# Performance work log

Measured on AMD Instinct MI355X. Metric: run time of the kernel, lower is better.

The kernel has to match this reference:

```python
import jax, jax.numpy as jnp
import numpy as np

VOCAB = 31
SOS = 0  # VOCAB_MAP['<sos>']
B, T_ENC, T_DEC, D = 64, 1000, 300, 512


def setup_inputs() -> dict:
    key = jax.random.key(0)
    ks = jax.random.split(key, 18)
    s = 0.05
    n = lambda k, shp: jax.random.normal(k, shp, jnp.float32) * s
    return {
        "encoder_output": jax.random.normal(ks[0], (B, T_ENC, D), jnp.float32),
        "encoder_len": jax.random.randint(ks[1], (B,), 100, T_ENC + 1),
        "y": jax.random.randint(ks[2], (B, T_DEC), 0, VOCAB),
        "embedding": n(ks[3], (VOCAB, D)),
        "W_ih0": n(ks[4], (4 * D, 2 * D)),
        "W_hh0": n(ks[5], (4 * D, D)),
        "b_ih0": jnp.zeros((4 * D,), jnp.float32),
        "b_hh0": jnp.zeros((4 * D,), jnp.float32),
        "W_ih1": n(ks[6], (4 * D, D)),
        "W_hh1": n(ks[7], (4 * D, D)),
        "b_ih1": jnp.zeros((4 * D,), jnp.float32),
        "b_hh1": jnp.zeros((4 * D,), jnp.float32),
        "Wq": n(ks[8], (D, D)),
        "Wk": n(ks[9], (D, D)),
        "Wv": n(ks[10], (D, D)),
        "W_out": n(ks[11], (D, 2 * D)),
        "b_out": jnp.zeros((D,), jnp.float32),
        "b_char": jnp.zeros((VOCAB,), jnp.float32),
    }


def _lstm_cell(x, h, c, Wih, Whh, bih, bhh):
    # torch LSTMCell: gates = x@Wih^T + bih + h@Whh^T + bhh, chunk order i,f,g,o
    g = x @ Wih.T + bih + h @ Whh.T + bhh
    i, f, gg, o = jnp.split(g, 4, axis=-1)
    c2 = jax.nn.sigmoid(f) * c + jax.nn.sigmoid(i) * jnp.tanh(gg)
    h2 = jax.nn.sigmoid(o) * jnp.tanh(c2)
    return h2, c2


def reference(encoder_output, encoder_len, y, embedding, W_ih0, W_hh0, b_ih0,
              b_hh0, W_ih1, W_hh1, b_ih1, b_hh1, Wq, Wk, Wv, W_out, b_out,
              b_char):
    Bb, T_dec = y.shape
    T_enc = encoder_output.shape[1]
    Dd = embedding.shape[1]
    # precompute attention keys/values once (attender caches these)
    keys_ = encoder_output @ Wk   # [B, T_enc, D]
    vals_ = encoder_output @ Wv   # [B, T_enc, D]
    mask = jnp.arange(T_enc)[None, :] < encoder_len[:, None]  # [B, T_enc]
    scale = 1.0 / jnp.sqrt(jnp.asarray(Dd, jnp.float32))

    def step(carry, xs):
        h0, c0, h1, c1, ctx, prev = carry
        t, yt = xs
        # teacher forcing (ratio=1): y[:,t] for 0<t<T-1, else previous argmax
        sym = jnp.where((t > 0) & (t < T_dec - 1), yt, prev)
        emb = embedding[sym]                       # [B, D]
        x = jnp.concatenate([emb, ctx], axis=-1)   # [B, 2D]
        h0, c0 = _lstm_cell(x, h0, c0, W_ih0, W_hh0, b_ih0, b_hh0)
        h1, c1 = _lstm_cell(h0, h1, c1, W_ih1, W_hh1, b_ih1, b_hh1)
        q = h1 @ Wq                                # [B, D]
        e = jnp.einsum('bd,btd->bt', q, keys_) * scale
        e = jnp.where(mask, e, jnp.float32(-1e9))
        w = jax.nn.softmax(e, axis=-1)             # [B, T_enc]
        ctx = jnp.einsum('bt,btd->bd', w, vals_)   # [B, D]
        cdn = jnp.concatenate([h1, ctx], axis=-1)  # [B, 2D]
        hid = jax.nn.relu(cdn @ W_out.T + b_out)
        logits = hid @ embedding.T + b_char        # tied weights, [B, 31]
        prev = jnp.argmax(logits, axis=-1)
        return (h0, c0, h1, c1, ctx, prev), (logits, w)

    z = jnp.zeros((Bb, Dd), encoder_output.dtype)
    prev0 = jnp.full((Bb,), SOS, dtype=y.dtype)
    init = (z, z, z, z, z, prev0)
    ts = jnp.arange(T_dec)
    _, (logits, attn) = jax.lax.scan(step, init, (ts, y.T))
    raw_outputs = jnp.transpose(logits, (1, 0, 2))      # [B, T_dec, 31]
    attention_plot = jnp.transpose(attn, (1, 0, 2))     # [B, T_dec, T_enc]
    return raw_outputs, attention_plot
```

## Files before the change

kernel.cpp:

```cpp
#include <hip/hip_runtime.h>


typedef __attribute__((ext_vector_type(8))) short s8bf;
typedef __attribute__((ext_vector_type(4))) float f32x4;

#define SCALE_E 0.044194173824159216f
#define SWEEP_SLOTS 352
#define POLL_CAP 65536

struct Ptrs {
  const float* enc; const int* elen; const int* y;
  const float* emb;
  const float* Wih0; const float* Whh0; const float* bih0; const float* bhh0;
  const float* Wih1; const float* Whh1; const float* bih1; const float* bhh1;
  const float* Wq; const float* Wk; const float* Wv;
  const float* Wout; const float* bout; const float* bchar;
  unsigned short* kv;
  unsigned short* W0p;
  unsigned short* W1p;
  unsigned short* Wob;
  unsigned short* WkvT;
  unsigned short* embbf;
  float* b0p; float* b1p;
  unsigned short* h0b;
  unsigned short* h1b;
  unsigned short* hidb;
  unsigned short* embsel;
  float* c0s; float* c1s;
  float* ctxa;
  float* ebuf;
  float* sbuf;
  int* plan;
  int* flagA;
  float* out;
};

__device__ __forceinline__ unsigned short f2bf(float f) {
  unsigned u = __float_as_uint(f);
  u += 0x7fffu + ((u >> 16) & 1u);
  return (unsigned short)(u >> 16);
}
__device__ __forceinline__ float bf2f(unsigned short h) {
  return __uint_as_float(((unsigned)h) << 16);
}
__device__ __forceinline__ float sigm(float x) { return 1.f / (1.f + __expf(-x)); }

__device__ __forceinline__ void st_u32_sc(unsigned* p, unsigned v) {
  __hip_atomic_store(p, v, __ATOMIC_RELAXED, __HIP_MEMORY_SCOPE_AGENT);
}
__device__ __forceinline__ s8bf ld16_sc(const unsigned short* p) {
  union { unsigned long long u[2]; s8bf v; } w;
  w.u[0] = __hip_atomic_load((unsigned long long*)p, __ATOMIC_RELAXED,
                             __HIP_MEMORY_SCOPE_AGENT);
  w.u[1] = __hip_atomic_load((unsigned long long*)(p + 4), __ATOMIC_RELAXED,
                             __HIP_MEMORY_SCOPE_AGENT);
  return w.v;
}

__global__ void k_init(Ptrs P) {
  int g = blockIdx.x * 256 + threadIdx.x;
  for (int i = g; i < 32768; i += 65536) { P.c0s[i] = 0.f; P.c1s[i] = 0.f; }
  for (int i = g; i < 65536; i += 65536) {
    P.h0b[i] = 0; P.h1b[i] = 0; P.ctxa[i] = 0.f;
  }
  for (int i = g; i < 131072; i += 65536) P.ebuf[i] = 0.f;
  if (g < 128) P.sbuf[g] = 0.f;
  if (g < 64) P.flagA[g] = 0;
}

__global__ void k_prep(Ptrs P) {
  int bid = blockIdx.x, tid = threadIdx.x;
  for (int ri = 0; ri < 8; ++ri) {
    int gp = bid * 8 + ri;
    int r = (gp & 3) * 512 + (gp >> 2);
    for (int k = tid; k < 1536; k += 256)
      P.W0p[(size_t)gp * 1536 + k] =
          f2bf(k < 1024 ? P.Wih0[(size_t)r * 1024 + k] : P.Whh0[(size_t)r * 512 + (k - 1024)]);
    for (int k = tid; k < 1024; k += 256)
      P.W1p[(size_t)gp * 1024 + k] =
          f2bf(k < 512 ? P.Wih1[(size_t)r * 512 + k] : P.Whh1[(size_t)r * 512 + (k - 512)]);
    if (tid == 0) {
      P.b0p[gp] = P.bih0[r] + P.bhh0[r];
      P.b1p[gp] = P.bih1[r] + P.bhh1[r];
    }
  }
  for (int ri = 0; ri < 2; ++ri) {
    int n = bid * 2 + ri;
    for (int k = tid; k < 1024; k += 256)
      P.Wob[(size_t)n * 1024 + k] = f2bf(P.Wout[(size_t)n * 1024 + k]);
  }
  {
    int g = bid * 256 + tid;
    if (g < 31 * 512) P.embbf[g] = f2bf(P.emb[g]);
  }
  for (int ri = 0; ri < 4; ++ri) {
    int n = bid * 4 + ri;
    if (n < 512) {
      const float* wq = P.Wq + (size_t)n * 512;
      for (int k = tid; k < 512; k += 256) {
        const float* wk = P.Wk + (size_t)k * 512;
        float s0 = 0.f, s1 = 0.f, s2 = 0.f, s3 = 0.f;
        for (int j = 0; j < 512; j += 4) {
          f32x4 a = *(const f32x4*)(wk + j);
          f32x4 b = *(const f32x4*)(wq + j);
          s0 = fmaf(a[0], b[0], s0); s1 = fmaf(a[1], b[1], s1);
          s2 = fmaf(a[2], b[2], s2); s3 = fmaf(a[3], b[3], s3);
        }
        P.WkvT[(size_t)n * 512 + k] = f2bf((s0 + s1) + (s2 + s3));
      }
    } else {
      for (int k = tid; k < 512; k += 256)
        P.WkvT[(size_t)n * 512 + k] = f2bf(P.Wv[(size_t)k * 512 + (n - 512)]);
    }
  }
  if (bid == 0 && tid == 0) {
    int tot = 0;
    for (int b = 0; b < 64; ++b) {
      int l = P.elen[b]; if (l > 1000) l = 1000;
      tot += l;
    }
    int acc = 0;
    P.plan[0] = 0;
    for (int b = 0; b < 64; ++b) {
      int l = P.elen[b]; if (l > 1000) l = 1000;
      int nb = (int)(((long long)l * 288) / tot);
      if (nb < 1) nb = 1;
      acc += nb;
      P.plan[b + 1] = acc;
    }
  }
}

__global__ __launch_bounds__(1024) void k_kv(Ptrs P) {
  int bid = blockIdx.x, tid = threadIdx.x;
  int w = tid >> 6, ln = tid & 63;
  __shared__ unsigned short lds2[16][16][16];
  int mt = bid * 16 + w;
  bool valid = mt < 4000;
  s8bf afr[16];
  if (valid) {
    const float* ar = P.enc + (size_t)(mt * 16 + (ln & 15)) * 512 + ((ln >> 4) * 8);
    for (int ks = 0; ks < 16; ++ks) {
      f32x4 v0 = *(const f32x4*)(ar + ks * 32);
      f32x4 v1 = *(const f32x4*)(ar + ks * 32 + 4);
      s8bf a;
      a[0] = (short)f2bf(v0[0]); a[1] = (short)f2bf(v0[1]);
      a[2] = (short)f2bf(v0[2]); a[3] = (short)f2bf(v0[3]);
      a[4] = (short)f2bf(v1[0]); a[5] = (short)f2bf(v1[1]);
      a[6] = (short)f2bf(v1[2]); a[7] = (short)f2bf(v1[3]);
      afr[ks] = a;
    }
  }
  for (int nt = 0; nt < 64; ++nt) {
    if (valid) {
      f32x4 acc = {0.f, 0.f, 0.f, 0.f};
      const unsigned short* br = P.WkvT + (size_t)(nt * 16 + (ln & 15)) * 512 + ((ln >> 4) * 8);
      for (int ks = 0; ks < 16; ++ks) {
        s8bf b = *(const s8bf*)(br + ks * 32);
        acc = __builtin_amdgcn_mfma_f32_16x16x32_bf16(afr[ks], b, acc, 0, 0, 0);
      }
      for (int r = 0; r < 4; ++r)
        lds2[w][(ln >> 4) * 4 + r][ln & 15] = f2bf(acc[r]);
    }
    __syncthreads();
    if (valid && ln < 32) {
      int row = ln >> 1, half = ln & 1;
      s8bf v = *(const s8bf*)&lds2[w][row][half * 8];
      *(s8bf*)(P.kv + (size_t)(mt * 16 + row) * 1024 + nt * 16 + half * 8) = v;
    }
    __syncthreads();
  }
}

__device__ __forceinline__ void hid_phase(int j, int tid, int s, const Ptrs& P,
                                          float (*lds_g)[16][16]) {
  int w = tid >> 6, ln = tid & 63;
  int kq = w >> 2, mt = w & 3;
  int nt = j;
  int brow = mt * 16 + (ln & 15), koff = (ln >> 4) * 8;
  int par = s & 1;
  const unsigned short* bp = P.Wob + (size_t)(nt * 16 + (ln & 15)) * 1024 + kq * 512 + koff;
  f32x4 acc = {0.f, 0.f, 0.f, 0.f};
  if (kq == 0) {
    const unsigned short* ap = P.h1b + par * 32768 + (size_t)brow * 512 + koff;
    for (int ks = 0; ks < 16; ++ks) {
      s8bf af = *(const s8bf*)(ap + ks * 32);
      s8bf bf8 = *(const s8bf*)(bp + ks * 32);
      acc = __builtin_amdgcn_mfma_f32_16x16x32_bf16(af, bf8, acc, 0, 0, 0);
    }
  } else {
    float inv = 1.f / P.sbuf[par * 64 + brow];
    const float* ap = P.ctxa + par * 32768 + (size_t)brow * 512 + koff;
    for (int ks = 0; ks < 16; ++ks) {
      f32x4 v0 = *(const f32x4*)(ap + ks * 32);
      f32x4 v1 = *(const f32x4*)(ap + ks * 32 + 4);
      s8bf af;
      af[0] = (short)f2bf(v0[0] * inv); af[1] = (short)f2bf(v0[1] * inv);
      af[2] = (short)f2bf(v0[2] * inv); af[3] = (short)f2bf(v0[3] * inv);
      af[4] = (short)f2bf(v1[0] * inv); af[5] = (short)f2bf(v1[1] * inv);
      af[6] = (short)f2bf(v1[2] * inv); af[7] = (short)f2bf(v1[3] * inv);
      s8bf bf8 = *(const s8bf*)(bp + ks * 32);
      acc = __builtin_amdgcn_mfma_f32_16x16x32_bf16(af, bf8, acc, 0, 0, 0);
    }
  }
  for (int r = 0; r < 4; ++r)
    lds_g[w][(ln >> 4) * 4 + r][ln & 15] = acc[r];
  __syncthreads();
  for (int r = 0; r < 2; ++r) {
    int idx = r * 512 + tid;
    int mt2 = idx >> 8, rb = (idx >> 4) & 15, cc = idx & 15;
    float hsum = lds_g[mt2][rb][cc] + lds_g[4 + mt2][rb][cc];
    hsum += P.bout[nt * 16 + cc];
    hsum = fmaxf(hsum, 0.f);
    P.hidb[(size_t)(mt2 * 16 + rb) * 512 + nt * 16 + cc] = f2bf(hsum);
  }
}

__device__ __forceinline__ void logits_phase(int lb, int tid, int s, const Ptrs& P,
                                             bool do_argmax) {
  int w = tid >> 6, ln = tid & 63;
  if (w >= 8) return;
  int b = lb * 8 + w;
  float hv[8];
  s8bf hh = *(const s8bf*)(P.hidb + (size_t)b * 512 + ln * 8);
  for (int j = 0; j < 8; ++j) hv[j] = bf2f((unsigned short)hh[j]);
  float mx = -3.4e38f; int am = 0;
  for (int v = 0; v < 31; ++v) {
    s8bf ee = *(const s8bf*)(P.embbf + (size_t)v * 512 + ln * 8);
    float p = 0.f;
    for (int j = 0; j < 8; ++j) p = fmaf(bf2f((unsigned short)ee[j]), hv[j], p);
    for (int off = 32; off; off >>= 1) p += __shfl_down(p, off);
    if (ln == 0) {
      float lg = p + P.bchar[v];
      P.out[(size_t)b * 9300 + (size_t)s * 31 + v] = lg;
      if (lg > mx) { mx = lg; am = v; }
    }
  }
  if (do_argmax) {
    am = __shfl(am, 0);
    *(s8bf*)(P.embsel + (size_t)b * 512 + ln * 8) =
        *(const s8bf*)(P.embbf + (size_t)am * 512 + ln * 8);
  }
}

__device__ __forceinline__ void attnnorm_phase(int j, int tid, int s, const Ptrs& P) {
  int idx = j * 512 + tid;
  if (idx >= 16000) return;
  int b = idx / 250, r = idx - b * 250;
  int par = s & 1;
  float inv = 1.f / P.sbuf[par * 64 + b];
  f32x4 v = *(const f32x4*)(P.ebuf + par * 65536 + b * 1024 + r * 4);
  v[0] *= inv; v[1] *= inv; v[2] *= inv; v[3] *= inv;
  *(f32x4*)(P.out + 595200 + (size_t)b * 300000 + (size_t)s * 1000 + r * 4) = v;
}

__global__ __launch_bounds__(512) void k_AB(Ptrs P, int t, int do_hid) {
  __shared__ float lds_g[8][16][16];
  __shared__ unsigned short lds_h0[16][520];
  int bid = blockIdx.x, tid = threadIdx.x;

  if (bid < 64) {
    int g = bid >> 4, s = bid & 15;
    int w = tid >> 6, ln = tid & 63;
    int nt = s * 8 + w;
    int brow = g * 16 + (ln & 15);
    int koff = (ln >> 4) * 8;
    int cur = t & 1, prv = cur ^ 1;

    const unsigned short* bp = P.W0p + (size_t)(nt * 16 + (ln & 15)) * 1536 + koff;
    f32x4 acc = {0.f, 0.f, 0.f, 0.f};
    {
      const unsigned short* embrow;
      if (t == 299) {
        embrow = P.embsel + (size_t)brow * 512 + koff;
      } else {
        int sym = (t == 0) ? 0 : P.y[brow * 300 + t];
        embrow = P.embbf + (size_t)sym * 512 + koff;
      }
      for (int ks = 0; ks < 16; ++ks) {
        s8bf af = *(const s8bf*)(embrow + ks * 32);
        s8bf bf8 = *(const s8bf*)(bp + ks * 32);
        acc = __builtin_amdgcn_mfma_f32_16x16x32_bf16(af, bf8, acc, 0, 0, 0);
      }
    }
    if (t > 0) {
      float inv = 1.f / P.sbuf[prv * 64 + brow];
      const float* cp = P.ctxa + prv * 32768 + (size_t)brow * 512 + koff;
      for (int ks = 0; ks < 16; ++ks) {
        f32x4 v0 = *(const f32x4*)(cp + ks * 32);
        f32x4 v1 = *(const f32x4*)(cp + ks * 32 + 4);
        s8bf af;
        af[0] = (short)f2bf(v0[0] * inv); af[1] = (short)f2bf(v0[1] * inv);
        af[2] = (short)f2bf(v0[2] * inv); af[3] = (short)f2bf(v0[3] * inv);
        af[4] = (short)f2bf(v1[0] * inv); af[5] = (short)f2bf(v1[1] * inv);
        af[6] = (short)f2bf(v1[2] * inv); af[7] = (short)f2bf(v1[3] * inv);
        s8bf bf8 = *(const s8bf*)(bp + 512 + ks * 32);
        acc = __builtin_amdgcn_mfma_f32_16x16x32_bf16(af, bf8, acc, 0, 0, 0);
      }
    }
    {
      const unsigned short* hp = P.h0b + prv * 32768 + (size_t)brow * 512 + koff;
      for (int ks = 0; ks < 16; ++ks) {
        s8bf af = *(const s8bf*)(hp + ks * 32);
        s8bf bf8 = *(const s8bf*)(bp + 1024 + ks * 32);
        acc = __builtin_amdgcn_mfma_f32_16x16x32_bf16(af, bf8, acc, 0, 0, 0);
      }
    }
    {
      float bias = P.b0p[nt * 16 + (ln & 15)];
      for (int r = 0; r < 4; ++r)
        lds_g[w][(ln >> 4) * 4 + r][ln & 15] = acc[r] + bias;
    }
    __syncthreads();
    {
      int tile = tid >> 6, rb = (tid >> 2) & 15, c = tid & 3;
      float gi = lds_g[tile][rb][4 * c + 0];
      float gf = lds_g[tile][rb][4 * c + 1];
      float gg = lds_g[tile][rb][4 * c + 2];
      float go = lds_g[tile][rb][4 * c + 3];
      int bb = g * 16 + rb, d = (s * 8 + tile) * 4 + c;
      float co = P.c0s[bb * 512 + d];
      float cn = fmaf(sigm(gf), co, sigm(gi) * tanhf(gg));
      float h = sigm(go) * tanhf(cn);
      P.c0s[bb * 512 + d] = cn;
      unsigned short hb = f2bf(h);
      int pr = __shfl_xor((int)(unsigned)hb, 1);
      if ((tid & 1) == 0)
        st_u32_sc((unsigned*)(P.h0b + cur * 32768 + bb * 512 + d),
                  ((unsigned)hb) | ((unsigned)pr << 16));
    }
    __syncthreads();

    if (tid == 0) {
      __hip_atomic_fetch_add(P.flagA + g * 16, 1, __ATOMIC_RELAXED,
                             __HIP_MEMORY_SCOPE_AGENT);
      int target = 16 * (t + 1);
      int gc = 0;
      while (__hip_atomic_load(P.flagA + g * 16, __ATOMIC_RELAXED,
                               __HIP_MEMORY_SCOPE_AGENT) < target) {
        if (++gc > POLL_CAP) break;
        __builtin_amdgcn_s_sleep(1);
      }
    }
    __syncthreads();

    {
      int bb2 = tid >> 5;
      int c0 = (tid & 31) * 16;
      const unsigned short* src = P.h0b + cur * 32768 + (size_t)(g * 16 + bb2) * 512 + c0;
      s8bf v0 = ld16_sc(src);
      s8bf v1 = ld16_sc(src + 8);
      *(s8bf*)&lds_h0[bb2][c0] = v0;
      *(s8bf*)&lds_h0[bb2][c0 + 8] = v1;
    }
    __syncthreads();

    const unsigned short* bp1 = P.W1p + (size_t)(nt * 16 + (ln & 15)) * 1024 + koff;
    f32x4 acc1 = {0.f, 0.f, 0.f, 0.f};
    for (int ks = 0; ks < 16; ++ks) {
      s8bf af = *(const s8bf*)&lds_h0[ln & 15][koff + ks * 32];
      s8bf bf8 = *(const s8bf*)(bp1 + ks * 32);
      acc1 = __builtin_amdgcn_mfma_f32_16x16x32_bf16(af, bf8, acc1, 0, 0, 0);
    }
    {
      const unsigned short* h1p = P.h1b + prv * 32768 + (size_t)brow * 512 + koff;
      for (int ks = 0; ks < 16; ++ks) {
        s8bf af = *(const s8bf*)(h1p + ks * 32);
        s8bf bf8 = *(const s8bf*)(bp1 + 512 + ks * 32);
        acc1 = __builtin_amdgcn_mfma_f32_16x16x32_bf16(af, bf8, acc1, 0, 0, 0);
      }
    }
    {
      float bias = P.b1p[nt * 16 + (ln & 15)];
      for (int r = 0; r < 4; ++r)
        lds_g[w][(ln >> 4) * 4 + r][ln & 15] = acc1[r] + bias;
    }
    __syncthreads();
    {
      int tile = tid >> 6, rb = (tid >> 2) & 15, c = tid & 3;
      float gi = lds_g[tile][rb][4 * c + 0];
      float gf = lds_g[tile][rb][4 * c + 1];
      float gg = lds_g[tile][rb][4 * c + 2];
      float go = lds_g[tile][rb][4 * c + 3];
      int bb = g * 16 + rb, d = (s * 8 + tile) * 4 + c;
      float co = P.c1s[bb * 512 + d];
      float cn = fmaf(sigm(gf), co, sigm(gi) * tanhf(gg));
      float h = sigm(go) * tanhf(cn);
      P.c1s[bb * 512 + d] = cn;
      unsigned short hb = f2bf(h);
      int pr = __shfl_xor((int)(unsigned)hb, 1);
      if ((tid & 1) == 0)
        *(unsigned*)(P.h1b + cur * 32768 + bb * 512 + d) =
            ((unsigned)hb) | ((unsigned)pr << 16);
    }
  } else if (bid < 96) {
    if (t > 0 && do_hid) hid_phase(bid - 64, tid, t - 1, P, lds_g);
  } else if (bid < 128) {
    if (t > 0) attnnorm_phase(bid - 96, tid, t - 1, P);
  } else {
    int idx = (bid - 128) * 512 + tid;
    f32x4 z = {0.f, 0.f, 0.f, 0.f};
    *(f32x4*)(P.ctxa + (t & 1) * 32768 + idx * 4) = z;
    if (bid == 128 && tid < 64) P.sbuf[(t & 1) * 64 + tid] = 0.f;
  }
}

__global__ __launch_bounds__(1024) void k_C(Ptrs P, int t, int do_logits) {
  __shared__ float lds_ctx[16][512];
  __shared__ float lds_s[16];
  __shared__ int lplan[65];
  int bid = blockIdx.x, tid = threadIdx.x;
  if (bid >= SWEEP_SLOTS) {
    if (do_logits) logits_phase(bid - SWEEP_SLOTS, tid, t - 1, P, false);
    return;
  }
  if (tid < 65) lplan[tid] = P.plan[tid];
  __syncthreads();
  if (bid >= lplan[64]) return;
  int lo = 0, hi = 64;
  while (lo + 1 < hi) { int mid = (lo + hi) >> 1; if (bid >= lplan[mid]) lo = mid; else hi = mid; }
  int b = lo;
  int nb = lplan[b + 1] - lplan[b];
  int ci = bid - lplan[b];
  int len = P.elen[b]; if (len > 1000) len = 1000;
  int per = (len + nb - 1) / nb;
  int t0 = ci * per;
  int lim = t0 + per; if (lim > len) lim = len;
  if (t0 >= lim) return;

  int w = tid >> 6, ln = tid & 63;
  int par = t & 1;
  float h1r[8];
  {
    s8bf hh = *(const s8bf*)(P.h1b + par * 32768 + (size_t)b * 512 + ln * 8);
    for (int j = 0; j < 8; ++j) h1r[j] = bf2f((unsigned short)hh[j]);
  }
  float acc[8] = {0.f, 0.f, 0.f, 0.f, 0.f, 0.f, 0.f, 0.f};
  float wsum = 0.f;
  float* eb = P.ebuf + par * 65536 + b * 1024;
  const unsigned short* kvb = P.kv + (size_t)b * 1000 * 1024;
  int tt = t0 + w;
  s8bf k0, v0, k1, v1;
  bool hv0 = tt < lim, hv1 = (tt + 16) < lim;
  if (hv0) {
    const unsigned short* r = kvb + (size_t)tt * 1024 + ln * 8;
    k0 = *(const s8bf*)r; v0 = *(const s8bf*)(r + 512);
  }
  if (hv1) {
    const unsigned short* r = kvb + (size_t)(tt + 16) * 1024 + ln * 8;
    k1 = *(const s8bf*)r; v1 = *(const s8bf*)(r + 512);
  }
  while (hv0) {
    s8bf k2, v2;
    bool hv2 = (tt + 32) < lim;
    if (hv2) {
      const unsigned short* r = kvb + (size_t)(tt + 32) * 1024 + ln * 8;
      k2 = *(const s8bf*)r; v2 = *(const s8bf*)(r + 512);
    }
    float p0 = 0.f, p1 = 0.f;
    for (int j = 0; j < 8; j += 2) {
      p0 = fmaf(bf2f((unsigned short)k0[j]), h1r[j], p0);
      p1 = fmaf(bf2f((unsigned short)k0[j + 1]), h1r[j + 1], p1);
    }
    float p = p0 + p1;
    p += __shfl_xor(p, 32); p += __shfl_xor(p, 16); p += __shfl_xor(p, 8);
    p += __shfl_xor(p, 4);  p += __shfl_xor(p, 2);  p += __shfl_xor(p, 1);
    float pe = __expf(p * SCALE_E);
    if (ln == 0) { eb[tt] = pe; wsum += pe; }
    for (int j = 0; j < 8; ++j)
      acc[j] = fmaf(bf2f((unsigned short)v0[j]), pe, acc[j]);
    k0 = k1; v0 = v1; hv0 = hv1;
    k1 = k2; v1 = v2; hv1 = hv2;
    tt += 16;
  }
  if (ln == 0) lds_s[w] = wsum;
  for (int j = 0; j < 8; ++j) lds_ctx[w][ln * 8 + j] = acc[j];
  __syncthreads();
  if (tid < 512) {
    float s = 0.f;
    for (int i = 0; i < 16; ++i) s += lds_ctx[i][tid];
    unsafeAtomicAdd(P.ctxa + par * 32768 + b * 512 + tid, s);
  }
  if (tid == 0) {
    float s = 0.f;
    for (int i = 0; i < 16; ++i) s += lds_s[i];
    unsafeAtomicAdd(P.sbuf + par * 64 + b, s);
  }
}

__global__ __launch_bounds__(512) void k_hid(Ptrs P, int t) {
  __shared__ float lds_g[8][16][16];
  hid_phase(blockIdx.x, threadIdx.x, t, P, lds_g);
}
__global__ __launch_bounds__(512) void k_logits(Ptrs P, int t, int do_argmax) {
  logits_phase(blockIdx.x, threadIdx.x, t, P, do_argmax != 0);
}
__global__ __launch_bounds__(512) void k_attn(Ptrs P, int t) {
  attnnorm_phase(blockIdx.x, threadIdx.x, t, P);
}

extern "C" void kernel_launch(void* const* d_in, const int* in_sizes, int n_in,
                              void* d_out, int out_size, void* d_ws, size_t ws_size,
                              hipStream_t stream) {
  (void)in_sizes; (void)n_in; (void)out_size; (void)ws_size;
  Ptrs P;
  P.enc   = (const float*)d_in[0];
  P.elen  = (const int*)d_in[1];
  P.y     = (const int*)d_in[2];
  P.emb   = (const float*)d_in[3];
  P.Wih0  = (const float*)d_in[4];
  P.Whh0  = (const float*)d_in[5];
  P.bih0  = (const float*)d_in[6];
  P.bhh0  = (const float*)d_in[7];
  P.Wih1  = (const float*)d_in[8];
  P.Whh1  = (const float*)d_in[9];
  P.bih1  = (const float*)d_in[10];
  P.bhh1  = (const float*)d_in[11];
  P.Wq    = (const float*)d_in[12];
  P.Wk    = (const float*)d_in[13];
  P.Wv    = (const float*)d_in[14];
  P.Wout  = (const float*)d_in[15];
  P.bout  = (const float*)d_in[16];
  P.bchar = (const float*)d_in[17];
  P.out   = (float*)d_out;

  char* ws = (char*)d_ws;
  size_t o = 0;
  auto alloc = [&](size_t n) { char* p = ws + o; o = (o + n + 255) & ~(size_t)255; return p; };
  P.kv     = (unsigned short*)alloc(64000ull * 1024 * 2);
  P.W0p    = (unsigned short*)alloc(2048ull * 1536 * 2);
  P.W1p    = (unsigned short*)alloc(2048ull * 1024 * 2);
  P.Wob    = (unsigned short*)alloc(512ull * 1024 * 2);
  P.WkvT   = (unsigned short*)alloc(1024ull * 512 * 2);
  P.embbf  = (unsigned short*)alloc(31ull * 512 * 2);
  P.b0p    = (float*)alloc(2048 * 4);
  P.b1p    = (float*)alloc(2048 * 4);
  P.h0b    = (unsigned short*)alloc(2ull * 64 * 512 * 2);
  P.h1b    = (unsigned short*)alloc(2ull * 64 * 512 * 2);
  P.hidb   = (unsigned short*)alloc(64ull * 512 * 2);
  P.embsel = (unsigned short*)alloc(64ull * 512 * 2);
  P.c0s    = (float*)alloc(64ull * 512 * 4);
  P.c1s    = (float*)alloc(64ull * 512 * 4);
  P.ctxa   = (float*)alloc(2ull * 64 * 512 * 4);
  P.ebuf   = (float*)alloc(2ull * 64 * 1024 * 4);
  P.sbuf   = (float*)alloc(2ull * 64 * 4);
  P.plan   = (int*)alloc(65 * 4);
  P.flagA  = (int*)alloc(64 * 4);

  k_init<<<dim3(256), dim3(256), 0, stream>>>(P);
  k_prep<<<dim3(256), dim3(256), 0, stream>>>(P);
  k_kv<<<dim3(256), dim3(1024), 0, stream>>>(P);

  for (int t = 0; t < 300; ++t) {
    k_AB<<<dim3(144), dim3(512), 0, stream>>>(P, t, (t == 299) ? 0 : 1);
    k_C<<<dim3(SWEEP_SLOTS + 8), dim3(1024), 0, stream>>>(
        P, t, (t > 0 && t != 299) ? 1 : 0);
    if (t == 298) {
      k_hid<<<dim3(32), dim3(512), 0, stream>>>(P, 298);
      k_logits<<<dim3(8), dim3(512), 0, stream>>>(P, 298, 1);
    }
  }
  k_hid<<<dim3(32), dim3(512), 0, stream>>>(P, 299);
  k_attn<<<dim3(32), dim3(512), 0, stream>>>(P, 299);
  k_logits<<<dim3(8), dim3(512), 0, stream>>>(P, 299, 0);
}
```

Measured before the change: 20.85 ms.

## Fuse per-step LSTM and attention sweep into one kernel with flag sync

Merges the two per-timestep launches (LSTM/hid block and attention sweep with logits) into a single 512-block kernel. Cross-block dependencies are now handled by device-scope flag polling: flagH gates the attention sweep on the h1 write, and flagHid gates logits on the hid write. Context/sum zeroing moves into the LSTM blocks, and attention blocks shrink to 512 threads with more slots. The aim is to halve launch overhead and let phases overlap, at the cost of spin-waiting blocks that rely on co-residency. Polls that hit the cap break out and could read stale data.

```diff
diff --git a/kernel.cpp b/kernel.cpp
--- a/kernel.cpp
+++ b/kernel.cpp
@@ -5,8 +5,8 @@
 typedef __attribute__((ext_vector_type(4))) float f32x4;
 
 #define SCALE_E 0.044194173824159216f
-#define SWEEP_SLOTS 352
-#define POLL_CAP 65536
+#define SWEEP_SLOTS 376
+#define POLL_CAP (1 << 19)
 
 struct Ptrs {
   const float* enc; const int* elen; const int* y;
@@ -31,7 +31,9 @@
   float* ebuf;
   float* sbuf;
   int* plan;
-  int* flagA;
+  int* flagL;
+  int* flagH;
+  int* flagHid;
   float* out;
 };
 
@@ -46,6 +48,9 @@
 __device__ __forceinline__ float sigm(float x) { return 1.f / (1.f + __expf(-x)); }
 
 __device__ __forceinline__ void st_u32_sc(unsigned* p, unsigned v) {
+  __hip_atomic_store(p, v, __ATOMIC_RELAXED, __HIP_MEMORY_SCOPE_AGENT);
+}
+__device__ __forceinline__ void st_f32_sc(float* p, float v) {
   __hip_atomic_store(p, v, __ATOMIC_RELAXED, __HIP_MEMORY_SCOPE_AGENT);
 }
 __device__ __forceinline__ s8bf ld16_sc(const unsigned short* p) {
@@ -56,6 +61,14 @@
                              __HIP_MEMORY_SCOPE_AGENT);
   return w.v;
 }
+__device__ __forceinline__ void pollge(const int* p, int need) {
+  int g = 0;
+  while (__hip_atomic_load((int*)p, __ATOMIC_RELAXED, __HIP_MEMORY_SCOPE_AGENT) < need) {
+    if (++g > POLL_CAP) break;
+    if (g < 16) __builtin_amdgcn_s_sleep(1);
+    else        __builtin_amdgcn_s_sleep(8);
+  }
+}
 
 __global__ void k_init(Ptrs P) {
   int g = blockIdx.x * 256 + threadIdx.x;
@@ -65,7 +78,8 @@
   }
   for (int i = g; i < 131072; i += 65536) P.ebuf[i] = 0.f;
   if (g < 128) P.sbuf[g] = 0.f;
-  if (g < 64) P.flagA[g] = 0;
+  if (g < 64) { P.flagL[g] = 0; P.flagH[g] = 0; }
+  if (g < 16) P.flagHid[g] = 0;
 }
 
 __global__ void k_prep(Ptrs P) {
@@ -123,7 +137,7 @@
     P.plan[0] = 0;
     for (int b = 0; b < 64; ++b) {
       int l = P.elen[b]; if (l > 1000) l = 1000;
-      int nb = (int)(((long long)l * 288) / tot);
+      int nb = (int)(((long long)l * 312) / tot);
       if (nb < 1) nb = 1;
       acc += nb;
       P.plan[b + 1] = acc;
@@ -212,7 +226,11 @@
     float hsum = lds_g[mt2][rb][cc] + lds_g[4 + mt2][rb][cc];
     hsum += P.bout[nt * 16 + cc];
     hsum = fmaxf(hsum, 0.f);
-    P.hidb[(size_t)(mt2 * 16 + rb) * 512 + nt * 16 + cc] = f2bf(hsum);
+    unsigned short hb = f2bf(hsum);
+    int pr = __shfl_xor((int)(unsigned)hb, 1);
+    if ((tid & 1) == 0)
+      st_u32_sc((unsigned*)(P.hidb + (size_t)(mt2 * 16 + rb) * 512 + nt * 16 + cc),
+                ((unsigned)hb) | ((unsigned)pr << 16));
   }
 }
 
@@ -222,7 +240,7 @@
   if (w >= 8) return;
   int b = lb * 8 + w;
   float hv[8];
-  s8bf hh = *(const s8bf*)(P.hidb + (size_t)b * 512 + ln * 8);
+  s8bf hh = ld16_sc(P.hidb + (size_t)b * 512 + ln * 8);
   for (int j = 0; j < 8; ++j) hv[j] = bf2f((unsigned short)hh[j]);
   float mx = -3.4e38f; int am = 0;
   for (int v = 0; v < 31; ++v) {
@@ -254,12 +272,14 @@
   *(f32x4*)(P.out + 595200 + (size_t)b * 300000 + (size_t)s * 1000 + r * 4) = v;
 }
 
-__global__ __launch_bounds__(512) void k_AB(Ptrs P, int t, int do_hid) {
-  __shared__ float lds_g[8][16][16];
-  __shared__ unsigned short lds_h0[16][520];
+__global__ __launch_bounds__(512, 4) void k_step(Ptrs P, int t, int do_hid,
+                                                 int do_logits) {
+  __shared__ __align__(16) char smem[24832];
   int bid = blockIdx.x, tid = threadIdx.x;
 
   if (bid < 64) {
+    float (*lds_g)[16][16] = (float (*)[16][16])smem;
+    unsigned short (*lds_h0)[520] = (unsigned short (*)[520])(smem + 8192);
     int g = bid >> 4, s = bid & 15;
     int w = tid >> 6, ln = tid & 63;
     int nt = s * 8 + w;
@@ -329,18 +349,17 @@
         st_u32_sc((unsigned*)(P.h0b + cur * 32768 + bb * 512 + d),
                   ((unsigned)hb) | ((unsigned)pr << 16));
     }
+    {
+      int bz = g * 16 + s;
+      st_f32_sc(P.ctxa + cur * 32768 + bz * 512 + tid, 0.f);
+      if (s == 0 && tid < 16) st_f32_sc(P.sbuf + cur * 64 + g * 16 + tid, 0.f);
+    }
     __syncthreads();
 
     if (tid == 0) {
-      __hip_atomic_fetch_add(P.flagA + g * 16, 1, __ATOMIC_RELAXED,
+      __hip_atomic_fetch_add(P.flagL + g * 16, 1, __ATOMIC_RELAXED,
                              __HIP_MEMORY_SCOPE_AGENT);
-      int target = 16 * (t + 1);
-      int gc = 0;
-      while (__hip_atomic_load(P.flagA + g * 16, __ATOMIC_RELAXED,
-                               __HIP_MEMORY_SCOPE_AGENT) < target) {
-        if (++gc > POLL_CAP) break;
-        __builtin_amdgcn_s_sleep(1);
-      }
+      pollge(P.flagL + g * 16, 16 * (t + 1));
     }
     __syncthreads();
 
@@ -390,101 +409,110 @@
       unsigned short hb = f2bf(h);
       int pr = __shfl_xor((int)(unsigned)hb, 1);
       if ((tid & 1) == 0)
-        *(unsigned*)(P.h1b + cur * 32768 + bb * 512 + d) =
-            ((unsigned)hb) | ((unsigned)pr << 16);
-    }
+        st_u32_sc((unsigned*)(P.h1b + cur * 32768 + bb * 512 + d),
+                  ((unsigned)hb) | ((unsigned)pr << 16));
+    }
+    __syncthreads();
+    if (tid == 0)
+      __hip_atomic_fetch_add(P.flagH + g * 16, 1, __ATOMIC_RELAXED,
+                             __HIP_MEMORY_SCOPE_AGENT);
+
   } else if (bid < 96) {
-    if (t > 0 && do_hid) hid_phase(bid - 64, tid, t - 1, P, lds_g);
+    if (t > 0 && do_hid) {
+      hid_phase(bid - 64, tid, t - 1, P, (float (*)[16][16])smem);
+      __syncthreads();
+      if (tid == 0)
+        __hip_atomic_fetch_add(P.flagHid, 1, __ATOMIC_RELAXED,
+                               __HIP_MEMORY_SCOPE_AGENT);
+    }
   } else if (bid < 128) {
     if (t > 0) attnnorm_phase(bid - 96, tid, t - 1, P);
+  } else if (bid < 136) {
+    if (t > 0 && do_logits) {
+      if (tid == 0) pollge(P.flagHid, 32 * t);
+      __syncthreads();
+      logits_phase(bid - 128, tid, t - 1, P, false);
+    }
   } else {
-    int idx = (bid - 128) * 512 + tid;
-    f32x4 z = {0.f, 0.f, 0.f, 0.f};
-    *(f32x4*)(P.ctxa + (t & 1) * 32768 + idx * 4) = z;
-    if (bid == 128 && tid < 64) P.sbuf[(t & 1) * 64 + tid] = 0.f;
-  }
-}
-
-__global__ __launch_bounds__(1024) void k_C(Ptrs P, int t, int do_logits) {
-  __shared__ float lds_ctx[16][512];
-  __shared__ float lds_s[16];
-  __shared__ int lplan[65];
-  int bid = blockIdx.x, tid = threadIdx.x;
-  if (bid >= SWEEP_SLOTS) {
-    if (do_logits) logits_phase(bid - SWEEP_SLOTS, tid, t - 1, P, false);
-    return;
-  }
-  if (tid < 65) lplan[tid] = P.plan[tid];
-  __syncthreads();
-  if (bid >= lplan[64]) return;
-  int lo = 0, hi = 64;
-  while (lo + 1 < hi) { int mid = (lo + hi) >> 1; if (bid >= lplan[mid]) lo = mid; else hi = mid; }
-  int b = lo;
-  int nb = lplan[b + 1] - lplan[b];
-  int ci = bid - lplan[b];
-  int len = P.elen[b]; if (len > 1000) len = 1000;
-  int per = (len + nb - 1) / nb;
-  int t0 = ci * per;
-  int lim = t0 + per; if (lim > len) lim = len;
-  if (t0 >= lim) return;
-
-  int w = tid >> 6, ln = tid & 63;
-  int par = t & 1;
-  float h1r[8];
-  {
-    s8bf hh = *(const s8bf*)(P.h1b + par * 32768 + (size_t)b * 512 + ln * 8);
-    for (int j = 0; j < 8; ++j) h1r[j] = bf2f((unsigned short)hh[j]);
-  }
-  float acc[8] = {0.f, 0.f, 0.f, 0.f, 0.f, 0.f, 0.f, 0.f};
-  float wsum = 0.f;
-  float* eb = P.ebuf + par * 65536 + b * 1024;
-  const unsigned short* kvb = P.kv + (size_t)b * 1000 * 1024;
-  int tt = t0 + w;
-  s8bf k0, v0, k1, v1;
-  bool hv0 = tt < lim, hv1 = (tt + 16) < lim;
-  if (hv0) {
-    const unsigned short* r = kvb + (size_t)tt * 1024 + ln * 8;
-    k0 = *(const s8bf*)r; v0 = *(const s8bf*)(r + 512);
-  }
-  if (hv1) {
-    const unsigned short* r = kvb + (size_t)(tt + 16) * 1024 + ln * 8;
-    k1 = *(const s8bf*)r; v1 = *(const s8bf*)(r + 512);
-  }
-  while (hv0) {
-    s8bf k2, v2;
-    bool hv2 = (tt + 32) < lim;
-    if (hv2) {
-      const unsigned short* r = kvb + (size_t)(tt + 32) * 1024 + ln * 8;
-      k2 = *(const s8bf*)r; v2 = *(const s8bf*)(r + 512);
-    }
-    float p0 = 0.f, p1 = 0.f;
-    for (int j = 0; j < 8; j += 2) {
-      p0 = fmaf(bf2f((unsigned short)k0[j]), h1r[j], p0);
-      p1 = fmaf(bf2f((unsigned short)k0[j + 1]), h1r[j + 1], p1);
-    }
-    float p = p0 + p1;
-    p += __shfl_xor(p, 32); p += __shfl_xor(p, 16); p += __shfl_xor(p, 8);
-    p += __shfl_xor(p, 4);  p += __shfl_xor(p, 2);  p += __shfl_xor(p, 1);
-    float pe = __expf(p * SCALE_E);
-    if (ln == 0) { eb[tt] = pe; wsum += pe; }
-    for (int j = 0; j < 8; ++j)
-      acc[j] = fmaf(bf2f((unsigned short)v0[j]), pe, acc[j]);
-    k0 = k1; v0 = v1; hv0 = hv1;
-    k1 = k2; v1 = v2; hv1 = hv2;
-    tt += 16;
-  }
-  if (ln == 0) lds_s[w] = wsum;
-  for (int j = 0; j < 8; ++j) lds_ctx[w][ln * 8 + j] = acc[j];
-  __syncthreads();
-  if (tid < 512) {
-    float s = 0.f;
-    for (int i = 0; i < 16; ++i) s += lds_ctx[i][tid];
-    unsafeAtomicAdd(P.ctxa + par * 32768 + b * 512 + tid, s);
-  }
-  if (tid == 0) {
-    float s = 0.f;
-    for (int i = 0; i < 16; ++i) s += lds_s[i];
-    unsafeAtomicAdd(P.sbuf + par * 64 + b, s);
+    float (*lds_ctx)[512] = (float (*)[512])smem;
+    float* lds_s = (float*)(smem + 16384);
+    int* lplan = (int*)(smem + 16448);
+    if (tid < 65) lplan[tid] = P.plan[tid];
+    __syncthreads();
+    int slot = bid - 136;
+    if (slot >= lplan[64]) return;
+    int lo = 0, hi = 64;
+    while (lo + 1 < hi) { int mid = (lo + hi) >> 1; if (slot >= lplan[mid]) lo = mid; else hi = mid; }
+    int b = lo;
+    int nb = lplan[b + 1] - lplan[b];
+    int ci = slot - lplan[b];
+    int len = P.elen[b]; if (len > 1000) len = 1000;
+    int per = (len + nb - 1) / nb;
+    int t0 = ci * per;
+    int lim = t0 + per; if (lim > len) lim = len;
+    if (t0 >= lim) return;
+
+    if (tid == 0) pollge(P.flagH + (b >> 4) * 16, 16 * (t + 1));
+    __syncthreads();
+
+    int w = tid >> 6, ln = tid & 63;
+    int par = t & 1;
+    float h1r[8];
+    {
+      s8bf hh = ld16_sc(P.h1b + par * 32768 + (size_t)b * 512 + ln * 8);
+      for (int j = 0; j < 8; ++j) h1r[j] = bf2f((unsigned short)hh[j]);
+    }
+    float acc[8] = {0.f, 0.f, 0.f, 0.f, 0.f, 0.f, 0.f, 0.f};
+    float wsum = 0.f;
+    float* eb = P.ebuf + par * 65536 + b * 1024;
+    const unsigned short* kvb = P.kv + (size_t)b * 1000 * 1024;
+    int tt = t0 + w;
+    s8bf k0, v0, k1, v1;
+    bool hv0 = tt < lim, hv1 = (tt + 8) < lim;
+    if (hv0) {
+      const unsigned short* r = kvb + (size_t)tt * 1024 + ln * 8;
+      k0 = *(const s8bf*)r; v0 = *(const s8bf*)(r + 512);
+    }
+    if (hv1) {
+      const unsigned short* r = kvb + (size_t)(tt + 8) * 1024 + ln * 8;
+      k1 = *(const s8bf*)r; v1 = *(const s8bf*)(r + 512);
+    }
+    while (hv0) {
+      s8bf k2, v2;
+      bool hv2 = (tt + 16) < lim;
+      if (hv2) {
+        const unsigned short* r = kvb + (size_t)(tt + 16) * 1024 + ln * 8;
+        k2 = *(const s8bf*)r; v2 = *(const s8bf*)(r + 512);
+      }
+      float p0 = 0.f, p1 = 0.f;
+      for (int j = 0; j < 8; j += 2) {
+        p0 = fmaf(bf2f((unsigned short)k0[j]), h1r[j], p0);
+        p1 = fmaf(bf2f((unsigned short)k0[j + 1]), h1r[j + 1], p1);
+      }
+      float p = p0 + p1;
+      p += __shfl_xor(p, 32); p += __shfl_xor(p, 16); p += __shfl_xor(p, 8);
+      p += __shfl_xor(p, 4);  p += __shfl_xor(p, 2);  p += __shfl_xor(p, 1);
+      float pe = __expf(p * SCALE_E);
+      if (ln == 0) { eb[tt] = pe; wsum += pe; }
+      for (int j = 0; j < 8; ++j)
+        acc[j] = fmaf(bf2f((unsigned short)v0[j]), pe, acc[j]);
+      k0 = k1; v0 = v1; hv0 = hv1;
+      k1 = k2; v1 = v2; hv1 = hv2;
+      tt += 8;
+    }
+    if (ln == 0) lds_s[w] = wsum;
+    for (int j = 0; j < 8; ++j) lds_ctx[w][ln * 8 + j] = acc[j];
+    __syncthreads();
+    {
+      float ssum = 0.f;
+      for (int i = 0; i < 8; ++i) ssum += lds_ctx[i][tid];
+      unsafeAtomicAdd(P.ctxa + par * 32768 + b * 512 + tid, ssum);
+    }
+    if (tid == 0) {
+      float ssum = 0.f;
+      for (int i = 0; i < 8; ++i) ssum += lds_s[i];
+      unsafeAtomicAdd(P.sbuf + par * 64 + b, ssum);
+    }
   }
 }
 
@@ -545,16 +573,17 @@
   P.ebuf   = (float*)alloc(2ull * 64 * 1024 * 4);
   P.sbuf   = (float*)alloc(2ull * 64 * 4);
   P.plan   = (int*)alloc(65 * 4);
-  P.flagA  = (int*)alloc(64 * 4);
+  P.flagL  = (int*)alloc(64 * 4);
+  P.flagH  = (int*)alloc(64 * 4);
+  P.flagHid= (int*)alloc(16 * 4);
 
   k_init<<<dim3(256), dim3(256), 0, stream>>>(P);
   k_prep<<<dim3(256), dim3(256), 0, stream>>>(P);
   k_kv<<<dim3(256), dim3(1024), 0, stream>>>(P);
 
   for (int t = 0; t < 300; ++t) {
-    k_AB<<<dim3(144), dim3(512), 0, stream>>>(P, t, (t == 299) ? 0 : 1);
-    k_C<<<dim3(SWEEP_SLOTS + 8), dim3(1024), 0, stream>>>(
-        P, t, (t > 0 && t != 299) ? 1 : 0);
+    int last = (t == 299);
+    k_step<<<dim3(512), dim3(512), 0, stream>>>(P, t, last ? 0 : 1, last ? 0 : 1);
     if (t == 298) {
       k_hid<<<dim3(32), dim3(512), 0, stream>>>(P, 298);
       k_logits<<<dim3(8), dim3(512), 0, stream>>>(P, 298, 1);
```

Result: faster. 18.02 ms (-13.5%).
